# Performance work log

Hardware: AMD Instinct MI355X
Metric: run time of the kernel (lower is better)

## Reference

```python
import jax, jax.numpy as jnp
import numpy as np

D_MODEL = 256
NUM_HEADS = 4
EPS = 1e-6


def setup_inputs() -> dict:
    key = jax.random.key(0)
    ks = jax.random.split(key, 9)
    B, T, D = 4, 2048, D_MODEL
    scale = 1.0 / np.sqrt(D)
    inp = {
        "x": jax.random.normal(ks[0], (B, T, D), dtype=jnp.float32),
        "Wq": jax.random.normal(ks[1], (D, D), dtype=jnp.float32) * scale,
        "bq": jnp.zeros((D,), dtype=jnp.float32),
        "Wk": jax.random.normal(ks[2], (D, D), dtype=jnp.float32) * scale,
        "bk": jnp.zeros((D,), dtype=jnp.float32),
        "Wv": jax.random.normal(ks[3], (D, D), dtype=jnp.float32) * scale,
        "bv": jnp.zeros((D,), dtype=jnp.float32),
        "Wo": jax.random.normal(ks[4], (D, D), dtype=jnp.float32) * scale,
        "bo": jnp.zeros((D,), dtype=jnp.float32),
    }
    return inp


def _feature_map(a):
    # F.elu(x) + 1.0
    return jax.nn.elu(a) + 1.0


def reference(x, Wq, bq, Wk, bk, Wv, bv, Wo, bo):
    B, T, D = x.shape
    H = NUM_HEADS
    dh = D // H
    Q = _feature_map((x @ Wq + bq).reshape(B, T, H, dh))
    K = _feature_map((x @ Wk + bk).reshape(B, T, H, dh))
    V = (x @ Wv + bv).reshape(B, T, H, dh)
    # outer-product state: (B,T,H,dh,dh), cumulative over time
    KV = jnp.einsum('bthd,bthm->bthdm', K, V)
    S = jnp.cumsum(KV, axis=1)
    Z = jnp.cumsum(K, axis=1)
    out = jnp.einsum('bthd,bthdm->bthm', Q, S)
    denom = jnp.einsum('bthd,bthd->bth', Q, Z)[..., None] + EPS
    out = (out / denom).reshape(B, T, D)
    return out @ Wo + bo
```

## Files before the change

kernel.cpp:

```cpp
#include <hip/hip_runtime.h>
#include <hip/hip_bf16.h>

#define D_MODEL 256
#define NHEADS 4
#define DHEAD 64
#define BATCH 4
#define TSEQ 2048
#define CHUNK 64
#define NCHUNK (TSEQ / CHUNK)
#define NTOK (BATCH * TSEQ)
#define NBH (BATCH * NHEADS)
#define EPSV 1e-6f
#define LSTRF 68
#define PSTR 36

typedef __bf16 bf16x8 __attribute__((ext_vector_type(8)));
typedef float f32x4 __attribute__((ext_vector_type(4)));
typedef unsigned short us8 __attribute__((ext_vector_type(8)));

__device__ __forceinline__ float elu1(float a) {
    return a > 0.0f ? a + 1.0f : __expf(a);
}

__device__ __forceinline__ unsigned short f2bf(float f) {
    __hip_bfloat16 h = __float2bfloat16(f);
    return __builtin_bit_cast(unsigned short, h);
}

__device__ __forceinline__ float bf2f(unsigned short u) {
    return __bfloat162float(__builtin_bit_cast(__hip_bfloat16, u));
}

__device__ __forceinline__ void unpack2(unsigned int u, float& lo, float& hi) {
    lo = __builtin_bit_cast(float, u << 16);
    hi = __builtin_bit_cast(float, u & 0xFFFF0000u);
}

__device__ __forceinline__ void unpack8(uint4 u, float* f) {
    unpack2(u.x, f[0], f[1]);
    unpack2(u.y, f[2], f[3]);
    unpack2(u.z, f[4], f[5]);
    unpack2(u.w, f[6], f[7]);
}

__device__ __forceinline__ unsigned int pack2(float a, float b) {
    return (unsigned int)f2bf(a) | ((unsigned int)f2bf(b) << 16);
}

__device__ __forceinline__ bf16x8 frag8(const float* p) {
    const float4 x = *reinterpret_cast<const float4*>(p);
    const float4 y = *reinterpret_cast<const float4*>(p + 4);
    us8 u;
    u[0] = f2bf(x.x); u[1] = f2bf(x.y); u[2] = f2bf(x.z); u[3] = f2bf(x.w);
    u[4] = f2bf(y.x); u[5] = f2bf(y.y); u[6] = f2bf(y.z); u[7] = f2bf(y.w);
    return __builtin_bit_cast(bf16x8, u);
}

__device__ __forceinline__ void gld_lds16(const void* g, void* l) {
    __builtin_amdgcn_global_load_lds(
        (const __attribute__((address_space(1))) void*)g,
        (__attribute__((address_space(3))) void*)l, 16, 0, 0);
}

__global__ __launch_bounds__(256) void convert_kernel(
    const float* __restrict__ x,
    const float* __restrict__ Wq, const float* __restrict__ Wk,
    const float* __restrict__ Wv, const float* __restrict__ Wo,
    unsigned short* __restrict__ xb,
    unsigned short* __restrict__ Wt, unsigned short* __restrict__ Wot)
{
    const int tid = threadIdx.x;
    if (blockIdx.x < NTOK * D_MODEL / 8 / 256) {
        const int i = (blockIdx.x * 256 + tid) * 8;
        const float4 a = *reinterpret_cast<const float4*>(&x[i]);
        const float4 b = *reinterpret_cast<const float4*>(&x[i + 4]);
        ushort4 u0 = { f2bf(a.x), f2bf(a.y), f2bf(a.z), f2bf(a.w) };
        ushort4 u1 = { f2bf(b.x), f2bf(b.y), f2bf(b.z), f2bf(b.w) };
        *reinterpret_cast<ushort4*>(&xb[i]) = u0;
        *reinterpret_cast<ushort4*>(&xb[i + 4]) = u1;
        return;
    }
    __shared__ float Ls[64][65];
    const int bid = blockIdx.x - NTOK * D_MODEL / 8 / 256;
    const int wi = bid >> 4;
    const int ti = bid & 15;
    const int k0 = (ti >> 2) * 64, n0 = (ti & 3) * 64;
    const float* W = wi == 0 ? Wq : wi == 1 ? Wk : wi == 2 ? Wv : Wo;
#pragma unroll
    for (int i = 0; i < 16; ++i) {
        const int idx = i * 256 + tid;
        const int r = idx >> 6, c = idx & 63;
        Ls[r][c] = W[(size_t)(k0 + r) * D_MODEL + n0 + c];
    }
    __syncthreads();
    unsigned short* outp = (wi < 3) ? (Wt + (size_t)(wi * 256 + n0) * D_MODEL + k0)
                                    : (Wot + (size_t)n0 * D_MODEL + k0);
#pragma unroll
    for (int i = 0; i < 16; ++i) {
        const int idx = i * 256 + tid;
        const int rn = idx >> 6, ck = idx & 63;
        outp[(size_t)rn * D_MODEL + ck] = f2bf(Ls[ck][rn]);
    }
}

template<int MODE>
__global__ __launch_bounds__(256) void mfma_gemm_kernel(
    const unsigned short* __restrict__ A,
    const unsigned short* __restrict__ Bt,
    const float* __restrict__ b0, const float* __restrict__ b1,
    const float* __restrict__ b2,
    void* __restrict__ O0, void* __restrict__ O1, void* __restrict__ O2)
{
    __shared__ __align__(16) unsigned short As[128 * 64];
    __shared__ __align__(16) unsigned short Bs[128 * 64];
    const int tid = threadIdx.x;
    const int wave = tid >> 6, lane = tid & 63;
    const int la = lane & 15, q = lane >> 4;
    const int wm = (wave >> 1) * 64, wn = (wave & 1) * 64;

    int mtile, ntile;
    if (MODE == 0) { ntile = blockIdx.x % 6; mtile = blockIdx.x / 6; }
    else           { ntile = blockIdx.x & 1; mtile = blockIdx.x >> 1; }
    const int m0 = mtile * 128, n0 = ntile * 128;

    const unsigned short* Ab = A  + (size_t)m0 * D_MODEL;
    const unsigned short* Bb = Bt + (size_t)n0 * D_MODEL;

    f32x4 acc[4][4];
#pragma unroll
    for (int i = 0; i < 4; ++i)
#pragma unroll
        for (int j = 0; j < 4; ++j) acc[i][j] = (f32x4){0.f, 0.f, 0.f, 0.f};

    for (int k0 = 0; k0 < D_MODEL; k0 += 64) {
#pragma unroll
        for (int i = 0; i < 4; ++i) {
            const int bslot = i * 256 + wave * 64;
            const int slot = bslot + lane;
            const int m = slot >> 3, s = slot & 7;
            const int g = s ^ (m & 7);
            gld_lds16(Ab + (size_t)m * D_MODEL + k0 + g * 8, &As[bslot * 8]);
            gld_lds16(Bb + (size_t)m * D_MODEL + k0 + g * 8, &Bs[bslot * 8]);
        }
        __syncthreads();

        bf16x8 af[4][2], bfr[4][2];
#pragma unroll
        for (int i = 0; i < 4; ++i) {
#pragma unroll
            for (int kh = 0; kh < 2; ++kh) {
                const int g = kh * 4 + q;
                const int m = wm + i * 16 + la;
                af[i][kh] = *reinterpret_cast<const bf16x8*>(
                    &As[m * 64 + ((g ^ (m & 7)) << 3)]);
                const int n = wn + i * 16 + la;
                bfr[i][kh] = *reinterpret_cast<const bf16x8*>(
                    &Bs[n * 64 + ((g ^ (n & 7)) << 3)]);
            }
        }
#pragma unroll
        for (int mi = 0; mi < 4; ++mi)
#pragma unroll
            for (int ni = 0; ni < 4; ++ni) {
                acc[mi][ni] = __builtin_amdgcn_mfma_f32_16x16x32_bf16(
                    af[mi][0], bfr[ni][0], acc[mi][ni], 0, 0, 0);
                acc[mi][ni] = __builtin_amdgcn_mfma_f32_16x16x32_bf16(
                    af[mi][1], bfr[ni][1], acc[mi][ni], 0, 0, 0);
            }
        __syncthreads();
    }

#pragma unroll
    for (int mi = 0; mi < 4; ++mi) {
#pragma unroll
        for (int ni = 0; ni < 4; ++ni) {
            const int row = m0 + wm + mi * 16 + q * 4;
            const int col = n0 + wn + ni * 16 + la;
            if (MODE == 0) {
                const int which = col >> 8;
                const int cl = col & 255;
                unsigned short* Out = (unsigned short*)
                    (which == 0 ? O0 : which == 1 ? O1 : O2);
                const float* bias = which == 0 ? b0 : which == 1 ? b1 : b2;
                const int act = (which < 2);
                const float bv = bias[cl];
#pragma unroll
                for (int r = 0; r < 4; ++r) {
                    float v = acc[mi][ni][r] + bv;
                    if (act) v = elu1(v);
                    Out[(size_t)(row + r) * D_MODEL + cl] = f2bf(v);
                }
            } else {
                float* Out = (float*)O0;
                const float bv = b0[col];
#pragma unroll
                for (int r = 0; r < 4; ++r)
                    Out[(size_t)(row + r) * D_MODEL + col] = acc[mi][ni][r] + bv;
            }
        }
    }
}

__global__ __launch_bounds__(256) void chunksum_kernel(
    const unsigned short* __restrict__ Kb, const unsigned short* __restrict__ Vb,
    float* __restrict__ Pt, float* __restrict__ Zc)
{
    __shared__ __align__(16) float Ktf[DHEAD * LSTRF];
    __shared__ __align__(16) float Vtf[DHEAD * LSTRF];
    const int tid = threadIdx.x;
    const int c  = blockIdx.x % NCHUNK;
    const int bh = blockIdx.x / NCHUNK;
    const int b = bh / NHEADS, h = bh % NHEADS;
    const size_t gbase = ((size_t)(b * TSEQ + c * CHUNK)) * D_MODEL + h * DHEAD;

#pragma unroll
    for (int i = 0; i < 2; ++i) {
        const int idx = i * 256 + tid;
        const int t = idx >> 3, e0 = (idx & 7) * 8;
        float kf[8], vf[8];
        unpack8(*reinterpret_cast<const uint4*>(&Kb[gbase + (size_t)t * D_MODEL + e0]), kf);
        unpack8(*reinterpret_cast<const uint4*>(&Vb[gbase + (size_t)t * D_MODEL + e0]), vf);
#pragma unroll
        for (int j = 0; j < 8; ++j) {
            Ktf[(e0 + j) * LSTRF + t] = kf[j];
            Vtf[(e0 + j) * LSTRF + t] = vf[j];
        }
    }
    __syncthreads();

    const int wave = tid >> 6, lane = tid & 63;
    const int la = lane & 15, q = lane >> 4;
    const int wm = (wave >> 1) * 32, wn = (wave & 1) * 32;

    f32x4 acc[2][2];
#pragma unroll
    for (int i = 0; i < 2; ++i)
#pragma unroll
        for (int j = 0; j < 2; ++j) acc[i][j] = (f32x4){0.f, 0.f, 0.f, 0.f};

#pragma unroll
    for (int ks = 0; ks < 2; ++ks) {
        const int ko = ks * 32 + q * 8;
        const bf16x8 a0  = frag8(&Vtf[(wm + la) * LSTRF + ko]);
        const bf16x8 a1  = frag8(&Vtf[(wm + 16 + la) * LSTRF + ko]);
        const bf16x8 bb0 = frag8(&Ktf[(wn + la) * LSTRF + ko]);
        const bf16x8 bb1 = frag8(&Ktf[(wn + 16 + la) * LSTRF + ko]);
        acc[0][0] = __builtin_amdgcn_mfma_f32_16x16x32_bf16(a0, bb0, acc[0][0], 0, 0, 0);
        acc[0][1] = __builtin_amdgcn_mfma_f32_16x16x32_bf16(a0, bb1, acc[0][1], 0, 0, 0);
        acc[1][0] = __builtin_amdgcn_mfma_f32_16x16x32_bf16(a1, bb0, acc[1][0], 0, 0, 0);
        acc[1][1] = __builtin_amdgcn_mfma_f32_16x16x32_bf16(a1, bb1, acc[1][1], 0, 0, 0);
    }

    float* Pb = Pt + (size_t)blockIdx.x * (DHEAD * DHEAD);
#pragma unroll
    for (int mi = 0; mi < 2; ++mi)
#pragma unroll
        for (int ni = 0; ni < 2; ++ni) {
            const int row = wm + mi * 16 + q * 4;
            const int col = wn + ni * 16 + la;
#pragma unroll
            for (int r = 0; r < 4; ++r)
                Pb[(row + r) * DHEAD + col] = acc[mi][ni][r];
        }

    if (tid < DHEAD) {
        float z = 0.f;
        for (int t = 0; t < CHUNK; ++t) z += Ktf[tid * LSTRF + t];
        Zc[(size_t)blockIdx.x * DHEAD + tid] = z;
    }
}

__global__ __launch_bounds__(256) void chunkout_kernel(
    const unsigned short* __restrict__ Qb, const unsigned short* __restrict__ Kb,
    const unsigned short* __restrict__ Vb,
    const float* __restrict__ Pt, const float* __restrict__ Zc,
    unsigned short* __restrict__ Ob)
{
    __shared__ __align__(16) float Qs[CHUNK * LSTRF];
    __shared__ __align__(16) float Ks[CHUNK * LSTRF];
    __shared__ __align__(16) float Vtf[DHEAD * LSTRF];
    __shared__ __align__(16) float At[CHUNK * LSTRF];
    __shared__ __align__(16) unsigned int Stp[DHEAD * PSTR];
    __shared__ float zsh[DHEAD];
    __shared__ float dnm[CHUNK];

    const int tid = threadIdx.x;
    const int c  = blockIdx.x % NCHUNK;
    const int bh = blockIdx.x / NCHUNK;
    const int b = bh / NHEADS, h = bh % NHEADS;
    const size_t gbase = ((size_t)(b * TSEQ + c * CHUNK)) * D_MODEL + h * DHEAD;

#pragma unroll
    for (int i = 0; i < 2; ++i) {
        const int idx = i * 256 + tid;
        const int t = idx >> 3, e0 = (idx & 7) * 8;
        float qf[8], kf[8], vf[8];
        unpack8(*reinterpret_cast<const uint4*>(&Qb[gbase + (size_t)t * D_MODEL + e0]), qf);
        unpack8(*reinterpret_cast<const uint4*>(&Kb[gbase + (size_t)t * D_MODEL + e0]), kf);
        unpack8(*reinterpret_cast<const uint4*>(&Vb[gbase + (size_t)t * D_MODEL + e0]), vf);
        *reinterpret_cast<float4*>(&Qs[t * LSTRF + e0])     = (float4){qf[0], qf[1], qf[2], qf[3]};
        *reinterpret_cast<float4*>(&Qs[t * LSTRF + e0 + 4]) = (float4){qf[4], qf[5], qf[6], qf[7]};
        *reinterpret_cast<float4*>(&Ks[t * LSTRF + e0])     = (float4){kf[0], kf[1], kf[2], kf[3]};
        *reinterpret_cast<float4*>(&Ks[t * LSTRF + e0 + 4]) = (float4){kf[4], kf[5], kf[6], kf[7]};
#pragma unroll
        for (int j = 0; j < 8; ++j)
            Vtf[(e0 + j) * LSTRF + t] = vf[j];
    }

    {
        const int r = tid >> 2, q16 = tid & 3;
        float sacc[16];
#pragma unroll
        for (int k = 0; k < 16; ++k) sacc[k] = 0.f;
        const float* Pb = Pt + (size_t)bh * NCHUNK * (DHEAD * DHEAD)
                             + r * DHEAD + q16 * 16;
        for (int cp = 0; cp < c; ++cp) {
            const float* src = Pb + (size_t)cp * (DHEAD * DHEAD);
#pragma unroll
            for (int k = 0; k < 4; ++k) {
                const float4 v = *reinterpret_cast<const float4*>(&src[k * 4]);
                sacc[k * 4 + 0] += v.x;
                sacc[k * 4 + 1] += v.y;
                sacc[k * 4 + 2] += v.z;
                sacc[k * 4 + 3] += v.w;
            }
        }
        uint4 pa, pb2;
        pa.x  = pack2(sacc[0],  sacc[1]);  pa.y  = pack2(sacc[2],  sacc[3]);
        pa.z  = pack2(sacc[4],  sacc[5]);  pa.w  = pack2(sacc[6],  sacc[7]);
        pb2.x = pack2(sacc[8],  sacc[9]);  pb2.y = pack2(sacc[10], sacc[11]);
        pb2.z = pack2(sacc[12], sacc[13]); pb2.w = pack2(sacc[14], sacc[15]);
        *reinterpret_cast<uint4*>(&Stp[r * PSTR + q16 * 8])     = pa;
        *reinterpret_cast<uint4*>(&Stp[r * PSTR + q16 * 8 + 4]) = pb2;
    }
    if (tid < DHEAD) {
        float z = 0.f;
        for (int cp = 0; cp < c; ++cp)
            z += Zc[((size_t)bh * NCHUNK + cp) * DHEAD + tid];
        zsh[tid] = z;
    }
    __syncthreads();

    const int wave = tid >> 6, lane = tid & 63;
    const int la = lane & 15, q = lane >> 4;
    const int wt = (wave >> 1) * 32, wn = (wave & 1) * 32;

    f32x4 acc[2][2];
#pragma unroll
    for (int i = 0; i < 2; ++i)
#pragma unroll
        for (int j = 0; j < 2; ++j) acc[i][j] = (f32x4){0.f, 0.f, 0.f, 0.f};
#pragma unroll
    for (int ks = 0; ks < 2; ++ks) {
        const int ko = ks * 32 + q * 8;
        const bf16x8 a0  = frag8(&Qs[(wt + la) * LSTRF + ko]);
        const bf16x8 a1  = frag8(&Qs[(wt + 16 + la) * LSTRF + ko]);
        const bf16x8 bb0 = frag8(&Ks[(wn + la) * LSTRF + ko]);
        const bf16x8 bb1 = frag8(&Ks[(wn + 16 + la) * LSTRF + ko]);
        acc[0][0] = __builtin_amdgcn_mfma_f32_16x16x32_bf16(a0, bb0, acc[0][0], 0, 0, 0);
        acc[0][1] = __builtin_amdgcn_mfma_f32_16x16x32_bf16(a0, bb1, acc[0][1], 0, 0, 0);
        acc[1][0] = __builtin_amdgcn_mfma_f32_16x16x32_bf16(a1, bb0, acc[1][0], 0, 0, 0);
        acc[1][1] = __builtin_amdgcn_mfma_f32_16x16x32_bf16(a1, bb1, acc[1][1], 0, 0, 0);
    }
#pragma unroll
    for (int mi = 0; mi < 2; ++mi)
#pragma unroll
        for (int ni = 0; ni < 2; ++ni) {
            const int t0 = wt + mi * 16 + q * 4;
            const int s  = wn + ni * 16 + la;
#pragma unroll
            for (int r = 0; r < 4; ++r)
                At[(t0 + r) * LSTRF + s] = (s <= t0 + r) ? acc[mi][ni][r] : 0.f;
        }
    __syncthreads();

    if (tid < CHUNK) {
        float dv = 0.f;
        for (int s = 0; s < CHUNK; ++s) dv += At[tid * LSTRF + s];
        for (int d = 0; d < DHEAD; ++d) dv = fmaf(Qs[tid * LSTRF + d], zsh[d], dv);
        dnm[tid] = dv + EPSV;
    }
    __syncthreads();

    f32x4 o[2][2];
#pragma unroll
    for (int i = 0; i < 2; ++i)
#pragma unroll
        for (int j = 0; j < 2; ++j) o[i][j] = (f32x4){0.f, 0.f, 0.f, 0.f};
#pragma unroll
    for (int ks = 0; ks < 2; ++ks) {
        const int ko = ks * 32 + q * 8;
        const bf16x8 a0  = frag8(&Qs[(wt + la) * LSTRF + ko]);
        const bf16x8 a1  = frag8(&Qs[(wt + 16 + la) * LSTRF + ko]);
        const bf16x8 bb0 = __builtin_bit_cast(bf16x8,
            *reinterpret_cast<const uint4*>(&Stp[(wn + la) * PSTR + ks * 16 + q * 4]));
        const bf16x8 bb1 = __builtin_bit_cast(bf16x8,
            *reinterpret_cast<const uint4*>(&Stp[(wn + 16 + la) * PSTR + ks * 16 + q * 4]));
        o[0][0] = __builtin_amdgcn_mfma_f32_16x16x32_bf16(a0, bb0, o[0][0], 0, 0, 0);
        o[0][1] = __builtin_amdgcn_mfma_f32_16x16x32_bf16(a0, bb1, o[0][1], 0, 0, 0);
        o[1][0] = __builtin_amdgcn_mfma_f32_16x16x32_bf16(a1, bb0, o[1][0], 0, 0, 0);
        o[1][1] = __builtin_amdgcn_mfma_f32_16x16x32_bf16(a1, bb1, o[1][1], 0, 0, 0);
    }
#pragma unroll
    for (int ks = 0; ks < 2; ++ks) {
        const int ko = ks * 32 + q * 8;
        const bf16x8 a0  = frag8(&At[(wt + la) * LSTRF + ko]);
        const bf16x8 a1  = frag8(&At[(wt + 16 + la) * LSTRF + ko]);
        const bf16x8 bb0 = frag8(&Vtf[(wn + la) * LSTRF + ko]);
        const bf16x8 bb1 = frag8(&Vtf[(wn + 16 + la) * LSTRF + ko]);
        o[0][0] = __builtin_amdgcn_mfma_f32_16x16x32_bf16(a0, bb0, o[0][0], 0, 0, 0);
        o[0][1] = __builtin_amdgcn_mfma_f32_16x16x32_bf16(a0, bb1, o[0][1], 0, 0, 0);
        o[1][0] = __builtin_amdgcn_mfma_f32_16x16x32_bf16(a1, bb0, o[1][0], 0, 0, 0);
        o[1][1] = __builtin_amdgcn_mfma_f32_16x16x32_bf16(a1, bb1, o[1][1], 0, 0, 0);
    }

#pragma unroll
    for (int mi = 0; mi < 2; ++mi)
#pragma unroll
        for (int ni = 0; ni < 2; ++ni) {
            const int t0 = wt + mi * 16 + q * 4;
            const int m  = wn + ni * 16 + la;
#pragma unroll
            for (int r = 0; r < 4; ++r) {
                const float v = o[mi][ni][r] / dnm[t0 + r];
                Ob[gbase + (size_t)(t0 + r) * D_MODEL + m] = f2bf(v);
            }
        }
}

extern "C" void kernel_launch(void* const* d_in, const int* in_sizes, int n_in,
                              void* d_out, int out_size, void* d_ws, size_t ws_size,
                              hipStream_t stream)
{
    const float* x  = (const float*)d_in[0];
    const float* Wq = (const float*)d_in[1];
    const float* bq = (const float*)d_in[2];
    const float* Wk = (const float*)d_in[3];
    const float* bk = (const float*)d_in[4];
    const float* Wv = (const float*)d_in[5];
    const float* bv = (const float*)d_in[6];
    const float* Wo = (const float*)d_in[7];
    const float* bo = (const float*)d_in[8];
    float* out = (float*)d_out;

    const size_t NE = (size_t)NTOK * D_MODEL;
    unsigned short* xb  = (unsigned short*)d_ws;
    unsigned short* Wt  = xb + NE;
    unsigned short* Wot = Wt + 768 * 256;
    unsigned short* Qb  = Wot + 256 * 256;
    unsigned short* Kb  = Qb + NE;
    unsigned short* Vb  = Kb + NE;
    unsigned short* Ob  = Vb + NE;
    float* P = (float*)(Ob + NE);
    float* Z = P + (size_t)NBH * NCHUNK * DHEAD * DHEAD;

    convert_kernel<<<NTOK * D_MODEL / 8 / 256 + 64, 256, 0, stream>>>(
        x, Wq, Wk, Wv, Wo, xb, Wt, Wot);
    mfma_gemm_kernel<0><<<(NTOK / 128) * 6, 256, 0, stream>>>(
        xb, Wt, bq, bk, bv, Qb, Kb, Vb);
    chunksum_kernel<<<NBH * NCHUNK, 256, 0, stream>>>(Kb, Vb, P, Z);
    chunkout_kernel<<<NBH * NCHUNK, 256, 0, stream>>>(Qb, Kb, Vb, P, Z, Ob);
    mfma_gemm_kernel<1><<<(NTOK / 128) * 2, 256, 0, stream>>>(
        Ob, Wot, bo, nullptr, nullptr, out, nullptr, nullptr);
}
```

Baseline: 124.4 us.

## Replace per-chunk quadratic prefix accumulation with a dedicated exclusive-scan kernel

Adds a prefix_kernel that turns the per-chunk KV and K-sum partials into exclusive prefix sums in place. chunkout then reads one precomputed state per chunk instead of re-summing every earlier chunk, which removes the O(NCHUNK^2) global reads. In exchange it adds a kernel launch and an extra read/write pass over P. The state matrix is now fetched straight from global memory inside the MFMA fragment loads rather than staged as bf16 in shared memory.

```diff
diff --git a/kernel.cpp b/kernel.cpp
--- a/kernel.cpp
+++ b/kernel.cpp
@@ -12,7 +12,6 @@
 #define NBH (BATCH * NHEADS)
 #define EPSV 1e-6f
 #define LSTRF 68
-#define PSTR 36
 
 typedef __bf16 bf16x8 __attribute__((ext_vector_type(8)));
 typedef float f32x4 __attribute__((ext_vector_type(4)));
@@ -41,10 +40,6 @@
     unpack2(u.y, f[2], f[3]);
     unpack2(u.z, f[4], f[5]);
     unpack2(u.w, f[6], f[7]);
-}
-
-__device__ __forceinline__ unsigned int pack2(float a, float b) {
-    return (unsigned int)f2bf(a) | ((unsigned int)f2bf(b) << 16);
 }
 
 __device__ __forceinline__ bf16x8 frag8(const float* p) {
@@ -270,17 +265,52 @@
     }
 }
 
+__global__ __launch_bounds__(256) void prefix_kernel(
+    float* __restrict__ P, float* __restrict__ Zc)
+{
+    const int tid = threadIdx.x;
+    if (blockIdx.x < NBH * 16) {
+        const int bh = blockIdx.x >> 4;
+        const int e = ((blockIdx.x & 15) << 8) + tid;
+        const size_t base = (size_t)bh * NCHUNK * (DHEAD * DHEAD) + e;
+        float v[NCHUNK];
+#pragma unroll
+        for (int c = 0; c < NCHUNK; ++c) v[c] = P[base + (size_t)c * (DHEAD * DHEAD)];
+        float s = 0.f;
+#pragma unroll
+        for (int c = 0; c < NCHUNK; ++c) {
+            const float t = v[c];
+            P[base + (size_t)c * (DHEAD * DHEAD)] = s;
+            s += t;
+        }
+    } else {
+        const int j = ((int)(blockIdx.x - NBH * 16) << 8) + tid;
+        if (j < NBH * DHEAD) {
+            const int bh = j >> 6, d = j & 63;
+            float v[NCHUNK];
+#pragma unroll
+            for (int c = 0; c < NCHUNK; ++c) v[c] = Zc[(bh * NCHUNK + c) * DHEAD + d];
+            float s = 0.f;
+#pragma unroll
+            for (int c = 0; c < NCHUNK; ++c) {
+                const float t = v[c];
+                Zc[(bh * NCHUNK + c) * DHEAD + d] = s;
+                s += t;
+            }
+        }
+    }
+}
+
 __global__ __launch_bounds__(256) void chunkout_kernel(
     const unsigned short* __restrict__ Qb, const unsigned short* __restrict__ Kb,
     const unsigned short* __restrict__ Vb,
-    const float* __restrict__ Pt, const float* __restrict__ Zc,
+    const float* __restrict__ Pt, const float* __restrict__ Zx,
     unsigned short* __restrict__ Ob)
 {
     __shared__ __align__(16) float Qs[CHUNK * LSTRF];
     __shared__ __align__(16) float Ks[CHUNK * LSTRF];
     __shared__ __align__(16) float Vtf[DHEAD * LSTRF];
     __shared__ __align__(16) float At[CHUNK * LSTRF];
-    __shared__ __align__(16) unsigned int Stp[DHEAD * PSTR];
     __shared__ float zsh[DHEAD];
     __shared__ float dnm[CHUNK];
 
@@ -289,6 +319,7 @@
     const int bh = blockIdx.x / NCHUNK;
     const int b = bh / NHEADS, h = bh % NHEADS;
     const size_t gbase = ((size_t)(b * TSEQ + c * CHUNK)) * D_MODEL + h * DHEAD;
+    const float* Pp = Pt + (size_t)blockIdx.x * (DHEAD * DHEAD);
 
 #pragma unroll
     for (int i = 0; i < 2; ++i) {
@@ -306,39 +337,8 @@
         for (int j = 0; j < 8; ++j)
             Vtf[(e0 + j) * LSTRF + t] = vf[j];
     }
-
-    {
-        const int r = tid >> 2, q16 = tid & 3;
-        float sacc[16];
-#pragma unroll
-        for (int k = 0; k < 16; ++k) sacc[k] = 0.f;
-        const float* Pb = Pt + (size_t)bh * NCHUNK * (DHEAD * DHEAD)
-                             + r * DHEAD + q16 * 16;
-        for (int cp = 0; cp < c; ++cp) {
-            const float* src = Pb + (size_t)cp * (DHEAD * DHEAD);
-#pragma unroll
-            for (int k = 0; k < 4; ++k) {
-                const float4 v = *reinterpret_cast<const float4*>(&src[k * 4]);
-                sacc[k * 4 + 0] += v.x;
-                sacc[k * 4 + 1] += v.y;
-                sacc[k * 4 + 2] += v.z;
-                sacc[k * 4 + 3] += v.w;
-            }
-        }
-        uint4 pa, pb2;
-        pa.x  = pack2(sacc[0],  sacc[1]);  pa.y  = pack2(sacc[2],  sacc[3]);
-        pa.z  = pack2(sacc[4],  sacc[5]);  pa.w  = pack2(sacc[6],  sacc[7]);
-        pb2.x = pack2(sacc[8],  sacc[9]);  pb2.y = pack2(sacc[10], sacc[11]);
-        pb2.z = pack2(sacc[12], sacc[13]); pb2.w = pack2(sacc[14], sacc[15]);
-        *reinterpret_cast<uint4*>(&Stp[r * PSTR + q16 * 8])     = pa;
-        *reinterpret_cast<uint4*>(&Stp[r * PSTR + q16 * 8 + 4]) = pb2;
-    }
-    if (tid < DHEAD) {
-        float z = 0.f;
-        for (int cp = 0; cp < c; ++cp)
-            z += Zc[((size_t)bh * NCHUNK + cp) * DHEAD + tid];
-        zsh[tid] = z;
-    }
+    if (tid < DHEAD)
+        zsh[tid] = Zx[((size_t)bh * NCHUNK + c) * DHEAD + tid];
     __syncthreads();
 
     const int wave = tid >> 6, lane = tid & 63;
@@ -392,10 +392,8 @@
         const int ko = ks * 32 + q * 8;
         const bf16x8 a0  = frag8(&Qs[(wt + la) * LSTRF + ko]);
         const bf16x8 a1  = frag8(&Qs[(wt + 16 + la) * LSTRF + ko]);
-        const bf16x8 bb0 = __builtin_bit_cast(bf16x8,
-            *reinterpret_cast<const uint4*>(&Stp[(wn + la) * PSTR + ks * 16 + q * 4]));
-        const bf16x8 bb1 = __builtin_bit_cast(bf16x8,
-            *reinterpret_cast<const uint4*>(&Stp[(wn + 16 + la) * PSTR + ks * 16 + q * 4]));
+        const bf16x8 bb0 = frag8(&Pp[(wn + la) * DHEAD + ko]);
+        const bf16x8 bb1 = frag8(&Pp[(wn + 16 + la) * DHEAD + ko]);
         o[0][0] = __builtin_amdgcn_mfma_f32_16x16x32_bf16(a0, bb0, o[0][0], 0, 0, 0);
         o[0][1] = __builtin_amdgcn_mfma_f32_16x16x32_bf16(a0, bb1, o[0][1], 0, 0, 0);
         o[1][0] = __builtin_amdgcn_mfma_f32_16x16x32_bf16(a1, bb0, o[1][0], 0, 0, 0);
@@ -459,6 +457,7 @@
     mfma_gemm_kernel<0><<<(NTOK / 128) * 6, 256, 0, stream>>>(
         xb, Wt, bq, bk, bv, Qb, Kb, Vb);
     chunksum_kernel<<<NBH * NCHUNK, 256, 0, stream>>>(Kb, Vb, P, Z);
+    prefix_kernel<<<NBH * 16 + 4, 256, 0, stream>>>(P, Z);
     chunkout_kernel<<<NBH * NCHUNK, 256, 0, stream>>>(Qb, Kb, Vb, P, Z, Ob);
     mfma_gemm_kernel<1><<<(NTOK / 128) * 2, 256, 0, stream>>>(
         Ob, Wot, bo, nullptr, nullptr, out, nullptr, nullptr);
```

New measurement: 115.4 us. -7.3%, faster.
